# Kernel tuning notes

Measured on AMD Instinct MI355X. Metric: run time of the kernel, lower is better.

Reference implementation:

```python
import jax, jax.numpy as jnp
import numpy as np

OUT_FEATURES = 4096
IN_FEATURES = 4096
GROUP_SIZE = 256
NUM_GROUPS = OUT_FEATURES * IN_FEATURES // GROUP_SIZE  # 65536


def setup_inputs() -> dict:
    key = jax.random.key(0)
    k1, k2, k3 = jax.random.split(key, 3)
    x = jax.random.normal(k1, (4, 2048, IN_FEATURES), dtype=jnp.float32)
    weight_packed = jax.random.randint(k2, (NUM_GROUPS, GROUP_SIZE // 2), 0, 256, dtype=jnp.int32)
    # params[..., 0] = scale, params[..., 1] = zero_point; keep scales small like real quant params
    weight_params = jax.random.uniform(k3, (NUM_GROUPS, 2), dtype=jnp.float32) * jnp.array([0.01, 0.1], dtype=jnp.float32)
    return {"x": x, "weight_packed": weight_packed, "weight_params": weight_params}


def _dequantize_4bit(weight_packed, weight_params):
    # weight_packed: [G, gs/2] bytes, two 4-bit values per byte (low nibble = even index)
    scales = weight_params[:, 0:1]  # [G, 1]
    zeros = weight_params[:, 1:2]   # [G, 1]
    low = (weight_packed & 15).astype(jnp.float32)          # even positions
    high = ((weight_packed >> 4) & 15).astype(jnp.float32)  # odd positions
    q = jnp.stack([low, high], axis=-1).reshape(weight_packed.shape[0], -1)  # [G, gs]
    return q * scales + zeros


def reference(x, weight_packed, weight_params):
    w = _dequantize_4bit(weight_packed, weight_params)  # [G, gs]
    w = w.reshape(-1)[: OUT_FEATURES * IN_FEATURES].reshape(OUT_FEATURES, IN_FEATURES)
    # F.linear(x, W) = x @ W.T
    return jnp.einsum("bsi,oi->bso", x, w)
```

## Files before the change

kernel.cpp:

```cpp
#include <hip/hip_runtime.h>
#include <hip/hip_bf16.h>


#define M_DIM 8192
#define N_DIM 4096
#define K_DIM 4096

typedef __bf16 bf16x8 __attribute__((ext_vector_type(8)));
typedef float f32x4 __attribute__((ext_vector_type(4)));
typedef unsigned short us8 __attribute__((ext_vector_type(8)));

__device__ __forceinline__ unsigned short f2bf_rne(float f) {
    unsigned int u = __builtin_bit_cast(unsigned int, f);
    u += 0x7FFFu + ((u >> 16) & 1u);
    return (unsigned short)(u >> 16);
}

__global__ void prep_kernel(const float* __restrict__ x,
                            const int* __restrict__ packed,
                            const float* __restrict__ params,
                            ushort* __restrict__ a,
                            ushort* __restrict__ w) {
    int b = blockIdx.x;
    if (b < 16384) {
        int j = b * 256 + threadIdx.x;
        float4 v0 = ((const float4*)x)[2 * j];
        float4 v1 = ((const float4*)x)[2 * j + 1];
        us8 o;
        o[0] = f2bf_rne(v0.x); o[1] = f2bf_rne(v0.y);
        o[2] = f2bf_rne(v0.z); o[3] = f2bf_rne(v0.w);
        o[4] = f2bf_rne(v1.x); o[5] = f2bf_rne(v1.y);
        o[6] = f2bf_rne(v1.z); o[7] = f2bf_rne(v1.w);
        ((us8*)a)[j] = o;
    } else {
        int j = (b - 16384) * 256 + threadIdx.x;
        int4 v = ((const int4*)packed)[j];
        int g = j >> 5;
        float s = params[2 * g], z = params[2 * g + 1];
        unsigned int o0, o1, o2, o3;
        o0 = (unsigned int)f2bf_rne((float)(v.x & 15) * s + z)
           | ((unsigned int)f2bf_rne((float)((v.x >> 4) & 15) * s + z) << 16);
        o1 = (unsigned int)f2bf_rne((float)(v.y & 15) * s + z)
           | ((unsigned int)f2bf_rne((float)((v.y >> 4) & 15) * s + z) << 16);
        o2 = (unsigned int)f2bf_rne((float)(v.z & 15) * s + z)
           | ((unsigned int)f2bf_rne((float)((v.z >> 4) & 15) * s + z) << 16);
        o3 = (unsigned int)f2bf_rne((float)(v.w & 15) * s + z)
           | ((unsigned int)f2bf_rne((float)((v.w >> 4) & 15) * s + z) << 16);
        ((uint4*)w)[j] = make_uint4(o0, o1, o2, o3);
    }
}

__global__ __launch_bounds__(256, 4) void gemm_bt(const ushort* __restrict__ A,
                                                  const ushort* __restrict__ B,
                                                  float* __restrict__ C) {
    __shared__ __bf16 lds_a[128 * 64];
    __shared__ __bf16 lds_b[128 * 64];

    const int tid  = threadIdx.x;
    const int w    = tid >> 6;
    const int lane = tid & 63;
    const int quad = lane >> 4;
    const int l16  = lane & 15;

    const int m0 = blockIdx.y * 128;
    const int n0 = blockIdx.x * 128;
    const int wm = (w >> 1) * 64;
    const int wn = (w & 1) * 64;

    f32x4 acc[4][4] = {};

    const int srow = tid >> 3;
    const int scol = ((tid & 7) ^ (srow & 7)) * 8;

    const ushort* aptr0 = A + (size_t)(m0 + srow) * K_DIM + scol;
    const ushort* bptr0 = B + (size_t)(n0 + srow) * K_DIM + scol;

    const int swz8 = l16 & 7;

    for (int k0 = 0; k0 < K_DIM; k0 += 64) {
#pragma unroll
        for (int rd = 0; rd < 4; ++rd) {
            __builtin_amdgcn_global_load_lds(
                (const __attribute__((address_space(1))) void*)(aptr0 + k0 + rd * 32 * K_DIM),
                (__attribute__((address_space(3))) void*)(lds_a + rd * 2048 + w * 512),
                16, 0, 0);
            __builtin_amdgcn_global_load_lds(
                (const __attribute__((address_space(1))) void*)(bptr0 + k0 + rd * 32 * K_DIM),
                (__attribute__((address_space(3))) void*)(lds_b + rd * 2048 + w * 512),
                16, 0, 0);
        }

        __syncthreads();

#pragma unroll
        for (int ks = 0; ks < 2; ++ks) {
            const int cq = ((ks << 2) + quad);
            bf16x8 af[4], bfv[4];
#pragma unroll
            for (int i = 0; i < 4; ++i) {
                af[i]  = *(const bf16x8*)&lds_a[(wm + i * 16 + l16) * 64 + (cq ^ swz8) * 8];
                bfv[i] = *(const bf16x8*)&lds_b[(wn + i * 16 + l16) * 64 + (cq ^ swz8) * 8];
            }
#pragma unroll
            for (int i = 0; i < 4; ++i)
#pragma unroll
                for (int j = 0; j < 4; ++j)
                    acc[i][j] = __builtin_amdgcn_mfma_f32_16x16x32_bf16(
                        af[i], bfv[j], acc[i][j], 0, 0, 0);
        }

        __syncthreads();
    }

    const int crow = m0 + wm + quad * 4;
    const int ccol = n0 + wn + l16;
#pragma unroll
    for (int i = 0; i < 4; ++i)
#pragma unroll
        for (int j = 0; j < 4; ++j)
#pragma unroll
            for (int r = 0; r < 4; ++r)
                C[(size_t)(crow + i * 16 + r) * N_DIM + ccol + j * 16] = acc[i][j][r];
}

__global__ void naive_kernel(const float* __restrict__ x, const int* __restrict__ packed,
                             const float* __restrict__ params, float* __restrict__ out) {
    int idx = blockIdx.x * blockDim.x + threadIdx.x;
    if (idx >= M_DIM * N_DIM) return;
    int m = idx / N_DIM, o = idx % N_DIM;
    const float* xr = x + (size_t)m * K_DIM;
    float sum = 0.f;
    for (int gi = 0; gi < K_DIM / 256; ++gi) {
        int g = o * (K_DIM / 256) + gi;
        float s = params[2 * g], z = params[2 * g + 1];
        const int* p = packed + (size_t)g * 128;
        const float* xx = xr + gi * 256;
        for (int j = 0; j < 128; ++j) {
            int v = p[j];
            sum += xx[2 * j]     * ((float)(v & 15) * s + z);
            sum += xx[2 * j + 1] * ((float)((v >> 4) & 15) * s + z);
        }
    }
    out[idx] = sum;
}

extern "C" void kernel_launch(void* const* d_in, const int* in_sizes, int n_in,
                              void* d_out, int out_size, void* d_ws, size_t ws_size,
                              hipStream_t stream) {
    const float* x      = (const float*)d_in[0];
    const int*   packed = (const int*)d_in[1];
    const float* params = (const float*)d_in[2];
    float* out = (float*)d_out;

    const size_t a_bytes = (size_t)M_DIM * K_DIM * 2;
    const size_t w_bytes = (size_t)N_DIM * K_DIM * 2;

    if (ws_size >= a_bytes + w_bytes) {
        ushort* Abf = (ushort*)d_ws;
        ushort* Wbf = (ushort*)((char*)d_ws + a_bytes);

        prep_kernel<<<24576, 256, 0, stream>>>(x, packed, params, Abf, Wbf);

        dim3 grid(N_DIM / 128, M_DIM / 128);
        gemm_bt<<<grid, 256, 0, stream>>>(Abf, Wbf, out);
    } else {
        int n = M_DIM * N_DIM;
        naive_kernel<<<(n + 255) / 256, 256, 0, stream>>>(x, packed, params, out);
    }
}
```

Measured before the change: 471.9 us.

## Rewrite GEMM as 256x256 tile, 8-wave, double-buffered LDS pipeline

The bf16 GEMM moves from 128x128 tiles with 4 waves to 256x256 tiles with 8 waves, each wave computing 128x64. The K-loop is double-buffered in 128KB of LDS, and global-to-LDS loads for later stages are interleaved with MFMA work, using barriers, manual vmcnt waits and s_setprio. A 1D grid with a remapped block order is added for L2 locality. The aim is to raise arithmetic intensity and hide load latency, at the cost of lower occupancy and more complex synchronisation.

```diff
diff --git a/kernel.cpp b/kernel.cpp
--- a/kernel.cpp
+++ b/kernel.cpp
@@ -50,77 +50,120 @@
     }
 }
 
-__global__ __launch_bounds__(256, 4) void gemm_bt(const ushort* __restrict__ A,
+__global__ __launch_bounds__(512, 2) void gemm_bt(const ushort* __restrict__ A,
                                                   const ushort* __restrict__ B,
                                                   float* __restrict__ C) {
-    __shared__ __bf16 lds_a[128 * 64];
-    __shared__ __bf16 lds_b[128 * 64];
+    __shared__ ushort lds[65536];
 
     const int tid  = threadIdx.x;
     const int w    = tid >> 6;
     const int lane = tid & 63;
     const int quad = lane >> 4;
     const int l16  = lane & 15;
-
-    const int m0 = blockIdx.y * 128;
-    const int n0 = blockIdx.x * 128;
-    const int wm = (w >> 1) * 64;
-    const int wn = (w & 1) * 64;
-
-    f32x4 acc[4][4] = {};
+    const int wm   = w >> 2;
+    const int wn   = w & 3;
+
+    const int bid = blockIdx.x;
+    const int sid = (bid & 7) * 64 + (bid >> 3);
+    const int by  = sid & 31;
+    const int bx  = sid >> 5;
+    const int m0  = by * 256;
+    const int n0  = bx * 256;
 
     const int srow = tid >> 3;
     const int scol = ((tid & 7) ^ (srow & 7)) * 8;
-
-    const ushort* aptr0 = A + (size_t)(m0 + srow) * K_DIM + scol;
-    const ushort* bptr0 = B + (size_t)(n0 + srow) * K_DIM + scol;
-
-    const int swz8 = l16 & 7;
-
-    for (int k0 = 0; k0 < K_DIM; k0 += 64) {
-#pragma unroll
-        for (int rd = 0; rd < 4; ++rd) {
+    const ushort* aS = A + (size_t)(m0 + srow) * K_DIM + scol;
+    const ushort* bS = B + (size_t)(n0 + srow) * K_DIM + scol;
+
+    f32x4 acc[8][4] = {};
+
+    auto stageA = [&](int t, int h) {
+        const int kc   = (t < 64 ? t : 63) * 64;
+        const int slot = ((t & 1) * 2 + h) * 8192;
+#pragma unroll
+        for (int l = 0; l < 2; ++l)
             __builtin_amdgcn_global_load_lds(
-                (const __attribute__((address_space(1))) void*)(aptr0 + k0 + rd * 32 * K_DIM),
-                (__attribute__((address_space(3))) void*)(lds_a + rd * 2048 + w * 512),
+                (const __attribute__((address_space(1))) void*)(aS + (size_t)(h * 128 + l * 64) * K_DIM + kc),
+                (__attribute__((address_space(3))) void*)(lds + slot + (l * 512 + w * 64) * 8),
                 16, 0, 0);
+    };
+    auto stageB = [&](int t, int h) {
+        const int kc   = (t < 64 ? t : 63) * 64;
+        const int slot = 32768 + ((t & 1) * 2 + h) * 8192;
+#pragma unroll
+        for (int l = 0; l < 2; ++l)
             __builtin_amdgcn_global_load_lds(
-                (const __attribute__((address_space(1))) void*)(bptr0 + k0 + rd * 32 * K_DIM),
-                (__attribute__((address_space(3))) void*)(lds_b + rd * 2048 + w * 512),
+                (const __attribute__((address_space(1))) void*)(bS + (size_t)(h * 128 + l * 64) * K_DIM + kc),
+                (__attribute__((address_space(3))) void*)(lds + slot + (l * 512 + w * 64) * 8),
                 16, 0, 0);
+    };
+
+    stageB(0, 0); stageB(0, 1); stageA(0, 0); stageA(0, 1); stageB(1, 0); stageB(1, 1);
+    asm volatile("s_waitcnt vmcnt(4)" ::: "memory");
+    __builtin_amdgcn_s_barrier();
+
+    const int aBase = wm * 8192;
+    const int bBase = 32768 + (wn >> 1) * 8192;
+    const int bR0   = (wn & 1) * 64;
+    const int swz8  = l16 & 7;
+
+#pragma unroll 1
+    for (int i = 0; i < 32; ++i) {
+#pragma unroll
+        for (int hh = 0; hh < 2; ++hh) {
+            const int tc  = 2 * i + hh;
+            const int buf = hh * 16384;
+            const int sa  = 2 * i + 1 + hh;
+            const int sb  = 2 * i + 2 + hh;
+            bf16x8 bf[4][2];
+#pragma unroll
+            for (int q = 0; q < 4; ++q) {
+                if (q == 0) {
+#pragma unroll
+                    for (int j = 0; j < 4; ++j)
+#pragma unroll
+                        for (int ks = 0; ks < 2; ++ks) {
+                            const int r = bR0 + j * 16 + l16;
+                            const int c = (ks * 4 + quad) ^ swz8;
+                            bf[j][ks] = *(const bf16x8*)&lds[bBase + buf + r * 64 + c * 8];
+                        }
+                }
+                bf16x8 af[2][2];
+#pragma unroll
+                for (int ii = 0; ii < 2; ++ii)
+#pragma unroll
+                    for (int ks = 0; ks < 2; ++ks) {
+                        const int r = q * 32 + ii * 16 + l16;
+                        const int c = (ks * 4 + quad) ^ swz8;
+                        af[ii][ks] = *(const bf16x8*)&lds[aBase + buf + r * 64 + c * 8];
+                    }
+                if (q < 2) stageA(sa, q); else stageB(sb, q - 2);
+                if (q == 3) asm volatile("s_waitcnt vmcnt(4)" ::: "memory");
+                __builtin_amdgcn_s_barrier();
+                __builtin_amdgcn_s_setprio(1);
+#pragma unroll
+                for (int ks = 0; ks < 2; ++ks)
+#pragma unroll
+                    for (int ii = 0; ii < 2; ++ii)
+#pragma unroll
+                        for (int j = 0; j < 4; ++j)
+                            acc[q * 2 + ii][j] = __builtin_amdgcn_mfma_f32_16x16x32_bf16(
+                                af[ii][ks], bf[j][ks], acc[q * 2 + ii][j], 0, 0, 0);
+                __builtin_amdgcn_s_setprio(0);
+                __builtin_amdgcn_s_barrier();
+            }
         }
-
-        __syncthreads();
-
-#pragma unroll
-        for (int ks = 0; ks < 2; ++ks) {
-            const int cq = ((ks << 2) + quad);
-            bf16x8 af[4], bfv[4];
-#pragma unroll
-            for (int i = 0; i < 4; ++i) {
-                af[i]  = *(const bf16x8*)&lds_a[(wm + i * 16 + l16) * 64 + (cq ^ swz8) * 8];
-                bfv[i] = *(const bf16x8*)&lds_b[(wn + i * 16 + l16) * 64 + (cq ^ swz8) * 8];
-            }
-#pragma unroll
-            for (int i = 0; i < 4; ++i)
-#pragma unroll
-                for (int j = 0; j < 4; ++j)
-                    acc[i][j] = __builtin_amdgcn_mfma_f32_16x16x32_bf16(
-                        af[i], bfv[j], acc[i][j], 0, 0, 0);
-        }
-
-        __syncthreads();
-    }
-
-    const int crow = m0 + wm + quad * 4;
-    const int ccol = n0 + wn + l16;
-#pragma unroll
-    for (int i = 0; i < 4; ++i)
+    }
+
+    const int crow = m0 + wm * 128 + quad * 4;
+    const int ccol = n0 + wn * 64 + l16;
+#pragma unroll
+    for (int rf = 0; rf < 8; ++rf)
 #pragma unroll
         for (int j = 0; j < 4; ++j)
 #pragma unroll
             for (int r = 0; r < 4; ++r)
-                C[(size_t)(crow + i * 16 + r) * N_DIM + ccol + j * 16] = acc[i][j][r];
+                C[(size_t)(crow + rf * 16 + r) * N_DIM + ccol + j * 16] = acc[rf][j][r];
 }
 
 __global__ void naive_kernel(const float* __restrict__ x, const int* __restrict__ packed,
@@ -161,8 +204,7 @@
 
         prep_kernel<<<24576, 256, 0, stream>>>(x, packed, params, Abf, Wbf);
 
-        dim3 grid(N_DIM / 128, M_DIM / 128);
-        gemm_bt<<<grid, 256, 0, stream>>>(Abf, Wbf, out);
+        gemm_bt<<<512, 512, 0, stream>>>(Abf, Wbf, out);
     } else {
         int n = M_DIM * N_DIM;
         naive_kernel<<<(n + 255) / 256, 256, 0, stream>>>(x, packed, params, out);
```

Result: faster. 461.1 us (-2.3%).
